# Optimization experiments

Hardware: AMD Instinct MI355X
Metric: run time of the kernel (lower is better)

Reference implementation:

```python
import jax, jax.numpy as jnp
import numpy as np

B, S, H = 2, 2048, 4096
NH, HD = 32, 128          # num attention heads, head dim (kv_channels)
KVH = 2                   # multi_query_group_num (KV heads)
ROT = HD // 2             # 64 rotary dims -> rope cache last-2 dim = 32
QKV = NH * HD + 2 * KVH * HD  # 4608


def apply_rope(x, rope):
    # x: [b, nh, s, hd]; rope: [b, s, ROT//2, 2]
    b, nh, s, hd = x.shape
    x_rot, x_pass = x[..., :ROT], x[..., ROT:]
    xs = x_rot.reshape(b, nh, s, ROT // 2, 2)
    rc = rope[:, :s].reshape(b, 1, s, ROT // 2, 2)
    out = jnp.stack([
        xs[..., 0] * rc[..., 0] - xs[..., 1] * rc[..., 1],
        xs[..., 1] * rc[..., 0] + xs[..., 0] * rc[..., 1],
    ], axis=-1).reshape(b, nh, s, ROT)
    return jnp.concatenate([out, x_pass], axis=-1)


def setup_inputs() -> dict:
    key = jax.random.key(0)
    ks = jax.random.split(key, 6)
    hidden_states = jax.random.normal(ks[0], (B, S, H), dtype=jnp.float32)
    rotary_pos_emb = jax.random.normal(ks[1], (B, S, ROT // 2, 2), dtype=jnp.float32)
    # causal mask: True = masked (strict upper triangle), matching module's ~tril
    causal = jnp.triu(jnp.ones((S, S), dtype=jnp.bool_), k=1)
    attention_mask = jnp.broadcast_to(causal[None, None], (B, 1, S, S))
    W_qkv = jax.random.normal(ks[2], (QKV, H), dtype=jnp.float32) * (1.0 / np.sqrt(H))
    b_qkv = jax.random.normal(ks[3], (QKV,), dtype=jnp.float32) * 0.02
    W_dense = jax.random.normal(ks[4], (H, NH * HD), dtype=jnp.float32) * (1.0 / np.sqrt(NH * HD))
    return {"hidden_states": hidden_states, "rotary_pos_emb": rotary_pos_emb,
            "attention_mask": attention_mask, "W_qkv": W_qkv, "b_qkv": b_qkv,
            "W_dense": W_dense}


def reference(hidden_states, rotary_pos_emb, attention_mask, W_qkv, b_qkv, W_dense):
    b, s, _ = hidden_states.shape
    mixed = hidden_states @ W_qkv.T + b_qkv  # [b, s, QKV]
    q, k, v = jnp.split(mixed, [NH * HD, NH * HD + KVH * HD], axis=-1)
    q = q.reshape(b, s, NH, HD).transpose(0, 2, 1, 3)   # [b, NH, s, hd]
    k = k.reshape(b, s, KVH, HD).transpose(0, 2, 1, 3)  # [b, KVH, s, hd]
    v = v.reshape(b, s, KVH, HD).transpose(0, 2, 1, 3)
    q = apply_rope(q, rotary_pos_emb)
    k = apply_rope(k, rotary_pos_emb)
    # GQA expand KV heads to NH
    rep = NH // KVH
    k = jnp.repeat(k, rep, axis=1)
    v = jnp.repeat(v, rep, axis=1)
    scale = 1.0 / np.sqrt(HD)
    scores = jnp.einsum('bhqd,bhkd->bhqk', q, k).astype(jnp.float32) * scale
    scores = jnp.where(attention_mask, -jnp.inf, scores)
    probs = jax.nn.softmax(scores, axis=-1).astype(v.dtype)
    ctx = jnp.einsum('bhqk,bhkd->bhqd', probs, v)       # [b, NH, s, hd]
    ctx = ctx.transpose(0, 2, 1, 3).reshape(b, s, NH * HD)
    return ctx @ W_dense.T
```

## Files before the change

### kernel.cpp

```cpp
#include <hip/hip_runtime.h>
#include <hip/hip_bf16.h>
#include <stdint.h>

#define Bb 2
#define Ss 2048
#define Hh 4096
#define NHh 32
#define HDd 128
#define KVHh 2

typedef __attribute__((ext_vector_type(8))) short bf16x8;
typedef __attribute__((ext_vector_type(4))) float f32x4;
typedef __attribute__((ext_vector_type(16))) float f32x16;
typedef __attribute__((ext_vector_type(4))) unsigned int u32x4;
typedef unsigned short u16;
typedef unsigned int u32;
typedef unsigned long long u64;

__device__ __forceinline__ u16 f2b(float f) {
  union { float f; u32 u; } v; v.f = f;
  u32 r = v.u + 0x7fffu + ((v.u >> 16) & 1u);
  return (u16)(r >> 16);
}
__device__ __forceinline__ float b2f(u16 h) {
  union { u32 u; float f; } v; v.u = ((u32)h) << 16;
  return v.f;
}

__device__ __forceinline__ u32 cvtpk(float lo, float hi_) {
  u32 r;
  asm("v_cvt_pk_bf16_f32 %0, %1, %2" : "=v"(r) : "v"(lo), "v"(hi_));
  return r;
}
__device__ __forceinline__ void plswap(u32& x, u32& y) {
  asm volatile("v_permlane32_swap_b32 %0, %1" : "+v"(x), "+v"(y));
}

__device__ __forceinline__ void gload_lds16(const u16* g, u16* l) {
  __builtin_amdgcn_global_load_lds(
      (const __attribute__((address_space(1))) u32*)(uintptr_t)g,
      (__attribute__((address_space(3))) u32*)(u32)(uintptr_t)l,
      16, 0, 0);
}

__global__ void cvt2_k(const float* __restrict__ a, u16* __restrict__ oa,
                       const float* __restrict__ b, u16* __restrict__ ob) {
  int i = blockIdx.x * blockDim.x + threadIdx.x;
  const float* src;
  u16* dst;
  int off;
  if (i < 4194304) { src = a; dst = oa; off = i; }
  else { src = b; dst = ob; off = i - 4194304; }
  int idx = off * 4;
  float4 v = *(const float4*)&src[idx];
  u64 pack = (u64)f2b(v.x) | ((u64)f2b(v.y) << 16) |
             ((u64)f2b(v.z) << 32) | ((u64)f2b(v.w) << 48);
  *(u64*)&dst[idx] = pack;
}

__global__ void cvtW_k(const float* __restrict__ in, u16* __restrict__ out) {
  int i = blockIdx.x * blockDim.x + threadIdx.x;
  int idx = i * 4;
  float4 v = *(const float4*)&in[idx];
  u64 pack = (u64)f2b(v.x) | ((u64)f2b(v.y) << 16) |
             ((u64)f2b(v.z) << 32) | ((u64)f2b(v.w) << 48);
  *(u64*)&out[idx] = pack;
}

__global__ void rope_k(u16* __restrict__ X, const float* __restrict__ rope, int nheads) {
  int i = blockIdx.x * blockDim.x + threadIdx.x;
  int p = i & 31;
  int s = (i >> 5) & (Ss - 1);
  int bh = i >> 16;
  if (bh >= Bb * nheads) return;
  int b = bh / nheads;
  size_t base = ((size_t)bh * Ss + s) * HDd + p * 2;
  u32 x01 = *(u32*)&X[base];
  float x0 = b2f((u16)(x01 & 0xffff));
  float x1 = b2f((u16)(x01 >> 16));
  float2 rc = *(const float2*)&rope[(((size_t)b * Ss + s) * 32 + p) * 2];
  float o0 = x0 * rc.x - x1 * rc.y;
  float o1 = x1 * rc.x + x0 * rc.y;
  u32 o = (u32)f2b(o0) | ((u32)f2b(o1) << 16);
  *(u32*)&X[base] = o;
}

template <int KK>
__device__ __forceinline__ void stage_tileA(const u16* __restrict__ gbase, u16* dst, int tid) {
#pragma unroll
  for (int li = 0; li < 2; ++li) {
    int t16 = li * 512 + tid;
    int rt = t16 >> 2, ct = t16 & 3;
    int cg = ct ^ ((rt >> 1) & 3);
    gload_lds16(gbase + (size_t)rt * KK + cg * 8, dst + t16 * 8);
  }
}
template <int KK>
__device__ __forceinline__ void stage_tileB(const u16* __restrict__ gbase, u16* dst, int tid) {
  int t16 = tid;
  int rt = t16 >> 2, ct = t16 & 3;
  int cg = ct ^ ((rt >> 1) & 3);
  gload_lds16(gbase + (size_t)rt * KK + cg * 8, dst + t16 * 8);
}

__device__ __forceinline__ bf16x8 frag128(const u16* buf, int row, int lk) {
  int ch = lk ^ ((row >> 1) & 3);
  return *(const bf16x8*)&buf[row * 32 + ch * 8];
}

template <int NN, int KK, int COLG, int EPI>
__global__ __launch_bounds__(512, 4) void gemm256x128(
    const u16* __restrict__ A, const u16* __restrict__ Bm,
    float* __restrict__ Cout, const float* __restrict__ bias,
    u16* __restrict__ Qb, u16* __restrict__ Kb, u16* __restrict__ Vb) {
  __shared__ u16 As[2][8192];
  __shared__ u16 Bs[2][4096];
  const int tid = threadIdx.x;
  const int wave = tid >> 6;
  const int lane = tid & 63;
  const int lr = lane & 15;
  const int lk = lane >> 4;
  const int wr = wave >> 1;
  const int wc = wave & 1;
  const int bid = blockIdx.x;
  const int xcd = bid & 7;
  const int local = bid >> 3;
  const int rlr = local / COLG;
  const int rlc = local - rlr * COLG;
  const int m0 = ((xcd >> 2) * 8 + rlr) * 256;
  const int n0 = ((xcd & 3) * COLG + rlc) * 128;
  const int NT = KK / 32;

  f32x4 acc[4][4];
#pragma unroll
  for (int i = 0; i < 4; ++i)
#pragma unroll
    for (int j = 0; j < 4; ++j) acc[i][j] = (f32x4){0.f, 0.f, 0.f, 0.f};

  const u16* Ab = A + (size_t)m0 * KK;
  const u16* Bb_ = Bm + (size_t)n0 * KK;

  stage_tileA<KK>(Ab, &As[0][0], tid);
  stage_tileB<KK>(Bb_, &Bs[0][0], tid);
  asm volatile("s_waitcnt vmcnt(0)");
  __syncthreads();

  int cur = 0;
  for (int t = 0; t < NT; ++t) {
    if (t + 1 < NT) {
      stage_tileA<KK>(Ab + (t + 1) * 32, &As[cur ^ 1][0], tid);
      stage_tileB<KK>(Bb_ + (t + 1) * 32, &Bs[cur ^ 1][0], tid);
      asm volatile("s_waitcnt vmcnt(3)");
    } else {
      asm volatile("s_waitcnt vmcnt(0)");
    }
    __builtin_amdgcn_s_barrier();
    __builtin_amdgcn_sched_barrier(0);

    bf16x8 af[4], bf[4];
#pragma unroll
    for (int mi = 0; mi < 4; ++mi)
      af[mi] = frag128(&As[cur][0], wr * 64 + mi * 16 + lr, lk);
#pragma unroll
    for (int ni = 0; ni < 4; ++ni)
      bf[ni] = frag128(&Bs[cur][0], wc * 64 + ni * 16 + lr, lk);
    asm volatile("s_waitcnt lgkmcnt(0)");
    __builtin_amdgcn_sched_barrier(0);
    __builtin_amdgcn_s_setprio(1);
#pragma unroll
    for (int mi = 0; mi < 4; ++mi)
#pragma unroll
      for (int ni = 0; ni < 4; ++ni)
        acc[mi][ni] = __builtin_amdgcn_mfma_f32_16x16x32_bf16(af[mi], bf[ni], acc[mi][ni], 0, 0, 0);
    __builtin_amdgcn_s_setprio(0);
    __builtin_amdgcn_s_barrier();
    cur ^= 1;
  }

  if constexpr (EPI == 0) {
#pragma unroll
    for (int mi = 0; mi < 4; ++mi)
#pragma unroll
      for (int ni = 0; ni < 4; ++ni) {
        int col = n0 + wc * 64 + ni * 16 + lr;
        int rowb = m0 + wr * 64 + mi * 16 + lk * 4;
#pragma unroll
        for (int j = 0; j < 4; ++j)
          Cout[(size_t)(rowb + j) * NN + col] = acc[mi][ni][j];
      }
  } else {
#pragma unroll
    for (int ni = 0; ni < 4; ++ni) {
      int n = n0 + wc * 64 + ni * 16 + lr;
      float bv = bias[n];
#pragma unroll
      for (int mi = 0; mi < 4; ++mi) {
        int mb = m0 + wr * 64 + mi * 16 + lk * 4;
#pragma unroll
        for (int j = 0; j < 4; ++j) {
          int m = mb + j;
          int bb = m >> 11;
          int ss = m & 2047;
          u16 hv = f2b(acc[mi][ni][j] + bv);
          if (n < 4096) {
            Qb[(((size_t)bb * NHh + (n >> 7)) * Ss + ss) * HDd + (n & 127)] = hv;
          } else if (n < 4352) {
            int idx2 = n - 4096;
            Kb[(((size_t)bb * KVHh + (idx2 >> 7)) * Ss + ss) * HDd + (idx2 & 127)] = hv;
          } else {
            int idx2 = n - 4352;
            Vb[(((size_t)bb * KVHh + (idx2 >> 7)) * Ss + ss) * HDd + (idx2 & 127)] = hv;
          }
        }
      }
    }
  }
}

__global__ __launch_bounds__(512, 2) void attn_k(
    const u16* __restrict__ Qb, const u16* __restrict__ Kb,
    const u16* __restrict__ Vb, const float* __restrict__ rope,
    u16* __restrict__ Ctx) {
  __shared__ u16 Kt[2][64 * 128];
  __shared__ u16 Vt[2][128 * 64];
  const int tid = threadIdx.x;
  const int w = tid >> 6;
  const int lane = tid & 63;
  const int l31 = lane & 31;
  const int hi = lane >> 5;
  const int h = blockIdx.y, b = blockIdx.z;
  const int hkv = h >> 4;
  const u16* Qp = Qb + ((size_t)(b * NHh + h)) * Ss * HDd;
  const u16* Kp = Kb + ((size_t)(b * KVHh + hkv)) * Ss * HDd;
  const u16* Vp = Vb + ((size_t)(b * KVHh + hkv)) * Ss * HDd;

  const float scale = 0.08838834764831845f;
  const float L2E = 1.4426950408889634f;

  for (int hp = 0; hp < 2; ++hp) {
    const int qt = hp == 0 ? (7 - (int)blockIdx.x) : (int)blockIdx.x;
    const int qs = qt * 256;
    const int qw = qs + w * 32;
    const int qrow = qw + l31;
    const int nt = qs / 64 + 4;

    bf16x8 qf[8];
#pragma unroll
    for (int ds = 0; ds < 8; ++ds)
      qf[ds] = *(const bf16x8*)&Qp[(size_t)qrow * HDd + ds * 16 + hi * 8];
#pragma unroll
    for (int ds = 0; ds < 4; ++ds) {
      bf16x8 q = qf[ds];
      bf16x8 o;
#pragma unroll
      for (int i = 0; i < 4; ++i) {
        int p = ds * 8 + hi * 4 + i;
        float2 rc = *(const float2*)&rope[(((size_t)b * Ss + qrow) * 32 + p) * 2];
        float x0 = b2f((u16)q[2 * i]), x1 = b2f((u16)q[2 * i + 1]);
        o[2 * i] = (short)f2b(x0 * rc.x - x1 * rc.y);
        o[2 * i + 1] = (short)f2b(x1 * rc.x + x0 * rc.y);
      }
      qf[ds] = o;
    }

    f32x16 accO[4];
#pragma unroll
    for (int i = 0; i < 4; ++i)
#pragma unroll
      for (int r = 0; r < 16; ++r) accO[i][r] = 0.f;
    float m_r = -3.0e38f, l_r = 0.f;

    {
#pragma unroll
      for (int i = 0; i < 2; ++i) {
        int slot = w * 2 + i;
        int r = slot * 4 + (lane >> 4);
        int p = lane & 15;
        int gc = (p & 8) | ((p ^ r) & 7);
        gload_lds16(Kp + (size_t)r * HDd + gc * 8, &Kt[0][slot * 512]);
      }
      bf16x8 v0 = *(const bf16x8*)&Vp[(size_t)lane * HDd + w * 16];
      bf16x8 v1 = *(const bf16x8*)&Vp[(size_t)lane * HDd + w * 16 + 8];
      u32x4 sv = __builtin_bit_cast(u32x4, (lane & 1) ? v0 : v1);
      u32x4 rv;
      rv.x = __shfl_xor(sv.x, 1); rv.y = __shfl_xor(sv.y, 1);
      rv.z = __shfl_xor(sv.z, 1); rv.w = __shfl_xor(sv.w, 1);
      bf16x8 recv = __builtin_bit_cast(bf16x8, rv);
      int kvp = lane >> 1;
#pragma unroll
      for (int i = 0; i < 8; ++i) {
        int d = w * 16 + (lane & 1) * 8 + i;
        u16 lo = (lane & 1) ? (u16)recv[i] : (u16)v0[i];
        u16 hb = (lane & 1) ? (u16)v1[i] : (u16)recv[i];
        u32 val = (u32)lo | ((u32)hb << 16);
        int cp = (kvp >> 2) ^ (d & 7);
        *(u32*)&Vt[0][d * 64 + cp * 8 + (kvp & 3) * 2] = val;
      }
    }
    __syncthreads();

    for (int t = 0; t < nt; ++t) {
      const int j0 = t * 64;
      const int cur = t & 1;
      const bool havenext = (t + 1 < nt);
      bf16x8 nv0, nv1;
      if (havenext) {
        const int j1 = j0 + 64;
#pragma unroll
        for (int i = 0; i < 2; ++i) {
          int slot = w * 2 + i;
          int r = slot * 4 + (lane >> 4);
          int p = lane & 15;
          int gc = (p & 8) | ((p ^ r) & 7);
          gload_lds16(Kp + (size_t)(j1 + r) * HDd + gc * 8, &Kt[cur ^ 1][slot * 512]);
        }
        nv0 = *(const bf16x8*)&Vp[(size_t)(j1 + lane) * HDd + w * 16];
        nv1 = *(const bf16x8*)&Vp[(size_t)(j1 + lane) * HDd + w * 16 + 8];
      }

      if (j0 <= qw + 31) {
        f32x16 aS[2];
#pragma unroll
        for (int a = 0; a < 2; ++a)
#pragma unroll
          for (int r = 0; r < 16; ++r) aS[a][r] = 0.f;
#pragma unroll
        for (int kvb = 0; kvb < 2; ++kvb) {
          int r = kvb * 32 + l31;
#pragma unroll
          for (int ds = 0; ds < 8; ++ds) {
            int c = ds * 2 + hi;
            int cp = (c & 8) | ((c ^ r) & 7);
            bf16x8 kf = *(const bf16x8*)&Kt[cur][r * 128 + cp * 8];
            aS[kvb] = __builtin_amdgcn_mfma_f32_32x32x16_bf16(kf, qf[ds], aS[kvb], 0, 0, 0);
          }
        }
        const bool needmask = (j0 + 63 > qw);
        float mx = -3.0e38f;
#pragma unroll
        for (int a = 0; a < 2; ++a)
#pragma unroll
          for (int r = 0; r < 16; ++r) {
            float s = aS[a][r] * scale;
            if (needmask) {
              int kv = j0 + a * 32 + (r & 3) + 8 * (r >> 2) + 4 * hi;
              s = (kv > qrow) ? -3.0e38f : s;
            }
            aS[a][r] = s;
            mx = fmaxf(mx, s);
          }
        mx = fmaxf(mx, __shfl_xor(mx, 32));
        if (!__all(mx - m_r <= 8.0f)) {
          float mnew = fmaxf(m_r, mx);
          float corr = __builtin_amdgcn_exp2f((m_r - mnew) * L2E);
          l_r *= corr;
#pragma unroll
          for (int i = 0; i < 4; ++i)
#pragma unroll
            for (int r = 0; r < 16; ++r) accO[i][r] *= corr;
          m_r = mnew;
        }
        float sum = 0.f;
#pragma unroll
        for (int a = 0; a < 2; ++a)
#pragma unroll
          for (int r = 0; r < 16; ++r) {
            float pe = __builtin_amdgcn_exp2f((aS[a][r] - m_r) * L2E);
            aS[a][r] = pe;
            sum += pe;
          }
        sum += __shfl_xor(sum, 32);
        l_r += sum;

        u32 cc0[2][4], cc1[2][4];
#pragma unroll
        for (int a = 0; a < 2; ++a)
#pragma unroll
          for (int g = 0; g < 4; ++g) {
            cc0[a][g] = cvtpk(aS[a][g * 4 + 0], aS[a][g * 4 + 1]);
            cc1[a][g] = cvtpk(aS[a][g * 4 + 2], aS[a][g * 4 + 3]);
          }
        bf16x8 pa[4];
#pragma unroll
        for (int ks = 0; ks < 4; ++ks) {
          int a = ks >> 1, g0 = (ks & 1) * 2;
          u32 w0 = cc0[a][g0], w2 = cc0[a][g0 + 1];
          u32 w1 = cc1[a][g0], w3 = cc1[a][g0 + 1];
          plswap(w0, w2);
          plswap(w1, w3);
          u32x4 tv; tv.x = w0; tv.y = w1; tv.z = w2; tv.w = w3;
          pa[ks] = __builtin_bit_cast(bf16x8, tv);
        }
#pragma unroll
        for (int dblk = 0; dblk < 4; ++dblk) {
          int d = dblk * 32 + l31;
#pragma unroll
          for (int ks = 0; ks < 4; ++ks) {
            int c = ks * 2 + hi;
            int cp = c ^ (d & 7);
            bf16x8 vf = *(const bf16x8*)&Vt[cur][d * 64 + cp * 8];
            accO[dblk] = __builtin_amdgcn_mfma_f32_32x32x16_bf16(vf, pa[ks], accO[dblk], 0, 0, 0);
          }
        }
      }

      if (havenext) {
        u32x4 sv = __builtin_bit_cast(u32x4, (lane & 1) ? nv0 : nv1);
        u32x4 rv;
        rv.x = __shfl_xor(sv.x, 1); rv.y = __shfl_xor(sv.y, 1);
        rv.z = __shfl_xor(sv.z, 1); rv.w = __shfl_xor(sv.w, 1);
        bf16x8 recv = __builtin_bit_cast(bf16x8, rv);
        int kvp = lane >> 1;
#pragma unroll
        for (int i = 0; i < 8; ++i) {
          int d = w * 16 + (lane & 1) * 8 + i;
          u16 lo = (lane & 1) ? (u16)recv[i] : (u16)nv0[i];
          u16 hb = (lane & 1) ? (u16)nv1[i] : (u16)recv[i];
          u32 val = (u32)lo | ((u32)hb << 16);
          int cp = (kvp >> 2) ^ (d & 7);
          *(u32*)&Vt[cur ^ 1][d * 64 + cp * 8 + (kvp & 3) * 2] = val;
        }
      }
      __syncthreads();
    }

    {
      float il = 1.0f / l_r;
      size_t rb = ((size_t)b * Ss + qrow) * (size_t)(NHh * HDd) + (size_t)h * HDd;
#pragma unroll
      for (int dblk = 0; dblk < 4; ++dblk)
#pragma unroll
        for (int g = 0; g < 4; ++g) {
          int d0 = dblk * 32 + g * 8 + hi * 4;
          u64 pack = (u64)f2b(accO[dblk][g * 4 + 0] * il) |
                     ((u64)f2b(accO[dblk][g * 4 + 1] * il) << 16) |
                     ((u64)f2b(accO[dblk][g * 4 + 2] * il) << 32) |
                     ((u64)f2b(accO[dblk][g * 4 + 3] * il) << 48);
          *(u64*)&Ctx[rb + d0] = pack;
        }
    }
    __syncthreads();
  }
}

extern "C" void kernel_launch(void* const* d_in, const int* in_sizes, int n_in,
                              void* d_out, int out_size, void* d_ws, size_t ws_size,
                              hipStream_t stream) {
  const float* hidden = (const float*)d_in[0];
  const float* rope = (const float*)d_in[1];
  const float* Wqkv = (const float*)d_in[3];
  const float* bqkv = (const float*)d_in[4];
  const float* Wdense = (const float*)d_in[5];
  float* out = (float*)d_out;

  char* w = (char*)d_ws;
  u16* Xbf = (u16*)w;
  u16* ctx = Xbf;
  w += (size_t)33554432;
  u16* Wq = (u16*)w;
  u16* Wd = Wq;
  w += (size_t)37748736;
  u16* Qb = (u16*)w; w += (size_t)33554432;
  u16* Kb = (u16*)w; w += (size_t)2097152;
  u16* Vb = (u16*)w; w += (size_t)2097152;

  cvt2_k<<<34816, 256, 0, stream>>>(hidden, Xbf, Wqkv, Wq);
  gemm256x128<4608, 4096, 9, 1><<<dim3(576), 512, 0, stream>>>(
      Xbf, Wq, nullptr, bqkv, Qb, Kb, Vb);
  rope_k<<<(Bb * KVHh * Ss * 32 + 255) / 256, 256, 0, stream>>>(Kb, rope, KVHh);
  cvtW_k<<<16384, 256, 0, stream>>>(Wdense, Wd);
  attn_k<<<dim3(4, NHh, Bb), 512, 0, stream>>>(Qb, Kb, Vb, rope, ctx);
  gemm256x128<4096, 4096, 8, 0><<<dim3(512), 512, 0, stream>>>(
      ctx, Wd, out, nullptr, nullptr, nullptr, nullptr);
}
```

Measured before the change: 490.5 us.

## Add deeper-pipelined dense output GEMM with BK=64 and triple-buffered A tiles

Splits the generic GEMM template into a QKV-specific kernel and a new dense-projection kernel. The new dense kernel uses a K-tile of 64, a three-slot ring buffer for A and a double buffer for B, and prefetches two tiles ahead. Each iteration is split into two MFMA halves so global-to-LDS loads interleave with compute. The aim is to halve the number of barrier-synchronised K iterations and hide memory latency better. The cost is much more LDS per block (about 128KB), which limits occupancy to fewer blocks per CU.

```diff
diff --git a/kernel.cpp b/kernel.cpp
--- a/kernel.cpp
+++ b/kernel.cpp
@@ -108,10 +108,10 @@
   return *(const bf16x8*)&buf[row * 32 + ch * 8];
 }
 
-template <int NN, int KK, int COLG, int EPI>
-__global__ __launch_bounds__(512, 4) void gemm256x128(
+template <int NN, int KK, int COLG>
+__global__ __launch_bounds__(512, 4) void gemm_qkv(
     const u16* __restrict__ A, const u16* __restrict__ Bm,
-    float* __restrict__ Cout, const float* __restrict__ bias,
+    const float* __restrict__ bias,
     u16* __restrict__ Qb, u16* __restrict__ Kb, u16* __restrict__ Vb) {
   __shared__ u16 As[2][8192];
   __shared__ u16 Bs[2][4096];
@@ -138,10 +138,10 @@
     for (int j = 0; j < 4; ++j) acc[i][j] = (f32x4){0.f, 0.f, 0.f, 0.f};
 
   const u16* Ab = A + (size_t)m0 * KK;
-  const u16* Bb_ = Bm + (size_t)n0 * KK;
+  const u16* Bw = Bm + (size_t)n0 * KK;
 
   stage_tileA<KK>(Ab, &As[0][0], tid);
-  stage_tileB<KK>(Bb_, &Bs[0][0], tid);
+  stage_tileB<KK>(Bw, &Bs[0][0], tid);
   asm volatile("s_waitcnt vmcnt(0)");
   __syncthreads();
 
@@ -149,7 +149,7 @@
   for (int t = 0; t < NT; ++t) {
     if (t + 1 < NT) {
       stage_tileA<KK>(Ab + (t + 1) * 32, &As[cur ^ 1][0], tid);
-      stage_tileB<KK>(Bb_ + (t + 1) * 32, &Bs[cur ^ 1][0], tid);
+      stage_tileB<KK>(Bw + (t + 1) * 32, &Bs[cur ^ 1][0], tid);
       asm volatile("s_waitcnt vmcnt(3)");
     } else {
       asm volatile("s_waitcnt vmcnt(0)");
@@ -177,44 +177,166 @@
     cur ^= 1;
   }
 
-  if constexpr (EPI == 0) {
-#pragma unroll
-    for (int mi = 0; mi < 4; ++mi)
-#pragma unroll
-      for (int ni = 0; ni < 4; ++ni) {
-        int col = n0 + wc * 64 + ni * 16 + lr;
-        int rowb = m0 + wr * 64 + mi * 16 + lk * 4;
-#pragma unroll
-        for (int j = 0; j < 4; ++j)
-          Cout[(size_t)(rowb + j) * NN + col] = acc[mi][ni][j];
-      }
-  } else {
+#pragma unroll
+  for (int ni = 0; ni < 4; ++ni) {
+    int n = n0 + wc * 64 + ni * 16 + lr;
+    float bv = bias[n];
+#pragma unroll
+    for (int mi = 0; mi < 4; ++mi) {
+      int mb = m0 + wr * 64 + mi * 16 + lk * 4;
+#pragma unroll
+      for (int j = 0; j < 4; ++j) {
+        int m = mb + j;
+        int bb = m >> 11;
+        int ss = m & 2047;
+        u16 hv = f2b(acc[mi][ni][j] + bv);
+        if (n < 4096) {
+          Qb[(((size_t)bb * NHh + (n >> 7)) * Ss + ss) * HDd + (n & 127)] = hv;
+        } else if (n < 4352) {
+          int idx2 = n - 4096;
+          Kb[(((size_t)bb * KVHh + (idx2 >> 7)) * Ss + ss) * HDd + (idx2 & 127)] = hv;
+        } else {
+          int idx2 = n - 4352;
+          Vb[(((size_t)bb * KVHh + (idx2 >> 7)) * Ss + ss) * HDd + (idx2 & 127)] = hv;
+        }
+      }
+    }
+  }
+}
+
+__global__ __launch_bounds__(512, 2) void gemm_dense8p(
+    const u16* __restrict__ A, const u16* __restrict__ Bm,
+    float* __restrict__ Cout) {
+  __shared__ u16 Ar[3][256 * 64];
+  __shared__ u16 Bd[2][128 * 64];
+  const int tid = threadIdx.x;
+  const int wave = tid >> 6;
+  const int lane = tid & 63;
+  const int lr = lane & 15;
+  const int lk = lane >> 4;
+  const int wr = wave >> 1;
+  const int wc = wave & 1;
+  const int bid = blockIdx.x;
+  const int xcd = bid & 7;
+  const int local = bid >> 3;
+  const int m0 = ((xcd >> 2) * 8 + (local >> 3)) * 256;
+  const int n0 = ((xcd & 3) * 8 + (local & 7)) * 128;
+
+  f32x4 acc[4][4];
+#pragma unroll
+  for (int i = 0; i < 4; ++i)
+#pragma unroll
+    for (int j = 0; j < 4; ++j) acc[i][j] = (f32x4){0.f, 0.f, 0.f, 0.f};
+
+  auto STAGE_A = [&](int j, int ring) {
+    if (j >= 64) return;
+#pragma unroll
+    for (int li = 0; li < 4; ++li) {
+      int t16 = li * 512 + tid;
+      int row = t16 >> 3, c = t16 & 7;
+      int cs = c ^ (row & 7);
+      gload_lds16(A + (size_t)(m0 + row) * 4096 + j * 64 + cs * 8,
+                  &Ar[ring][0] + t16 * 8);
+    }
+  };
+  auto STAGE_B = [&](int j) {
+    if (j >= 64) return;
+#pragma unroll
+    for (int li = 0; li < 2; ++li) {
+      int t16 = li * 512 + tid;
+      int row = t16 >> 3, c = t16 & 7;
+      int cs = c ^ (row & 7);
+      gload_lds16(Bm + (size_t)(n0 + row) * 4096 + j * 64 + cs * 8,
+                  &Bd[j & 1][0] + t16 * 8);
+    }
+  };
+
+  STAGE_A(0, 0); STAGE_B(0);
+  STAGE_A(1, 1); STAGE_B(1);
+  asm volatile("s_waitcnt vmcnt(6)");
+  __builtin_amdgcn_s_barrier();
+  __builtin_amdgcn_sched_barrier(0);
+
+  int ra = 0;
+  int ra2 = 2;
+  for (int kt = 0; kt < 64; ++kt) {
+    const u16* Acur = &Ar[ra][0];
+    const u16* Bt = &Bd[kt & 1][0];
+    auto rdA = [&](int r, int kk) {
+      int ch = (kk * 4 + lk) ^ (r & 7);
+      return *(const bf16x8*)&Acur[r * 64 + ch * 8];
+    };
+    auto rdB = [&](int r, int kk) {
+      int ch = (kk * 4 + lk) ^ (r & 7);
+      return *(const bf16x8*)&Bt[r * 64 + ch * 8];
+    };
+
+    bf16x8 bfr[4][2], af[2][2];
+#pragma unroll
+    for (int ni = 0; ni < 4; ++ni)
+#pragma unroll
+      for (int kk = 0; kk < 2; ++kk)
+        bfr[ni][kk] = rdB(wc * 64 + ni * 16 + lr, kk);
+#pragma unroll
+    for (int i = 0; i < 2; ++i)
+#pragma unroll
+      for (int kk = 0; kk < 2; ++kk)
+        af[i][kk] = rdA(wr * 64 + i * 16 + lr, kk);
+    STAGE_A(kt + 2, ra2);
+    __builtin_amdgcn_s_barrier();
+    asm volatile("s_waitcnt lgkmcnt(0)");
+    __builtin_amdgcn_sched_barrier(0);
+    __builtin_amdgcn_s_setprio(1);
+#pragma unroll
+    for (int i = 0; i < 2; ++i)
+#pragma unroll
+      for (int ni = 0; ni < 4; ++ni)
+#pragma unroll
+        for (int kk = 0; kk < 2; ++kk)
+          acc[i][ni] = __builtin_amdgcn_mfma_f32_16x16x32_bf16(af[i][kk], bfr[ni][kk], acc[i][ni], 0, 0, 0);
+    __builtin_amdgcn_s_setprio(0);
+    __builtin_amdgcn_s_barrier();
+
+#pragma unroll
+    for (int i = 0; i < 2; ++i)
+#pragma unroll
+      for (int kk = 0; kk < 2; ++kk)
+        af[i][kk] = rdA(wr * 64 + (2 + i) * 16 + lr, kk);
+    STAGE_B(kt + 2);
+    __builtin_amdgcn_s_barrier();
+    asm volatile("s_waitcnt lgkmcnt(0)");
+    __builtin_amdgcn_sched_barrier(0);
+    __builtin_amdgcn_s_setprio(1);
+#pragma unroll
+    for (int i = 0; i < 2; ++i)
+#pragma unroll
+      for (int ni = 0; ni < 4; ++ni)
+#pragma unroll
+        for (int kk = 0; kk < 2; ++kk)
+          acc[2 + i][ni] = __builtin_amdgcn_mfma_f32_16x16x32_bf16(af[i][kk], bfr[ni][kk], acc[2 + i][ni], 0, 0, 0);
+    __builtin_amdgcn_s_setprio(0);
+    if (kt < 62) {
+      asm volatile("s_waitcnt vmcnt(6)");
+    } else {
+      asm volatile("s_waitcnt vmcnt(0)");
+    }
+    __builtin_amdgcn_s_barrier();
+    __builtin_amdgcn_sched_barrier(0);
+
+    ra = (ra == 2) ? 0 : ra + 1;
+    ra2 = (ra2 == 2) ? 0 : ra2 + 1;
+  }
+
+#pragma unroll
+  for (int mi = 0; mi < 4; ++mi)
 #pragma unroll
     for (int ni = 0; ni < 4; ++ni) {
-      int n = n0 + wc * 64 + ni * 16 + lr;
-      float bv = bias[n];
-#pragma unroll
-      for (int mi = 0; mi < 4; ++mi) {
-        int mb = m0 + wr * 64 + mi * 16 + lk * 4;
-#pragma unroll
-        for (int j = 0; j < 4; ++j) {
-          int m = mb + j;
-          int bb = m >> 11;
-          int ss = m & 2047;
-          u16 hv = f2b(acc[mi][ni][j] + bv);
-          if (n < 4096) {
-            Qb[(((size_t)bb * NHh + (n >> 7)) * Ss + ss) * HDd + (n & 127)] = hv;
-          } else if (n < 4352) {
-            int idx2 = n - 4096;
-            Kb[(((size_t)bb * KVHh + (idx2 >> 7)) * Ss + ss) * HDd + (idx2 & 127)] = hv;
-          } else {
-            int idx2 = n - 4352;
-            Vb[(((size_t)bb * KVHh + (idx2 >> 7)) * Ss + ss) * HDd + (idx2 & 127)] = hv;
-          }
-        }
-      }
-    }
-  }
+      int col = n0 + wc * 64 + ni * 16 + lr;
+      int rowb = m0 + wr * 64 + mi * 16 + lk * 4;
+#pragma unroll
+      for (int j = 0; j < 4; ++j)
+        Cout[(size_t)(rowb + j) * 4096 + col] = acc[mi][ni][j];
+    }
 }
 
 __global__ __launch_bounds__(512, 2) void attn_k(
@@ -465,11 +587,10 @@
   u16* Vb = (u16*)w; w += (size_t)2097152;
 
   cvt2_k<<<34816, 256, 0, stream>>>(hidden, Xbf, Wqkv, Wq);
-  gemm256x128<4608, 4096, 9, 1><<<dim3(576), 512, 0, stream>>>(
-      Xbf, Wq, nullptr, bqkv, Qb, Kb, Vb);
+  gemm_qkv<4608, 4096, 9><<<dim3(576), 512, 0, stream>>>(
+      Xbf, Wq, bqkv, Qb, Kb, Vb);
   rope_k<<<(Bb * KVHh * Ss * 32 + 255) / 256, 256, 0, stream>>>(Kb, rope, KVHh);
   cvtW_k<<<16384, 256, 0, stream>>>(Wdense, Wd);
   attn_k<<<dim3(4, NHh, Bb), 512, 0, stream>>>(Qb, Kb, Vb, rope, ctx);
-  gemm256x128<4096, 4096, 8, 0><<<dim3(512), 512, 0, stream>>>(
-      ctx, Wd, out, nullptr, nullptr, nullptr, nullptr);
-}
+  gemm_dense8p<<<dim3(512), 512, 0, stream>>>(ctx, Wd, out);
+}
```

Result: no change. 483.2 us (-1.5%).
